# Kernel optimization log

Measured on AMD Instinct MI355X. Metric: run time of the kernel, lower is better.

## Reference

```python
import jax, jax.numpy as jnp
import numpy as np

B, S, D_IN, D_OUT, E, K = 4, 2048, 1024, 1024, 8, 2


def setup_inputs() -> dict:
    key = jax.random.key(0)
    ks = jax.random.split(key, 6)
    scale_in = 1.0 / np.sqrt(D_IN)
    return {
        "x": jax.random.normal(ks[0], (B, S, D_IN), dtype=jnp.float32),
        "gate_w": jax.random.uniform(ks[1], (E, D_IN), jnp.float32, -scale_in, scale_in),
        "gate_b": jax.random.uniform(ks[2], (E,), jnp.float32, -scale_in, scale_in),
        "expert_biases": jnp.zeros((E,), dtype=jnp.float32),
        "expert_w": jax.random.uniform(ks[3], (E, D_OUT, D_IN), jnp.float32, -scale_in, scale_in),
        "expert_b": jax.random.uniform(ks[4], (E, D_OUT), jnp.float32, -scale_in, scale_in),
    }


def reference(x, gate_w, gate_b, expert_biases, expert_w, expert_b):
    # Gating: sigmoid(Linear(x) + expert_biases), then top-k over experts
    gate_logits = jnp.einsum("bsd,ed->bse", x, gate_w) + gate_b + expert_biases
    gate_probs = jax.nn.sigmoid(gate_logits)
    top_k_probs, top_k_indices = jax.lax.top_k(gate_probs, K)  # [B,S,K]
    top_k_probs = top_k_probs / jnp.sum(top_k_probs, axis=-1, keepdims=True)

    # Dense all-expert compute: stack[e,b,s,o]
    expert_outputs = jnp.einsum("bsd,eod->ebso", x, expert_w) + expert_b[:, None, None, :]

    # Faithful reproduction of the original gather/permute:
    # result[b,s,j,o] = expert_outputs[tki[b,s,j], b, s, j]  (feature index is j, not o)
    bi = jnp.arange(B)[:, None, None]
    si = jnp.arange(S)[None, :, None]
    ji = jnp.arange(K)[None, None, :]
    val = expert_outputs[top_k_indices, bi, si, ji]  # [B,S,K]

    weighted = jnp.sum(val * top_k_probs, axis=-1)  # [B,S]
    final_output = jnp.broadcast_to(weighted[..., None], (B, S, D_OUT))
    return final_output, top_k_indices
```

## Files before the change

kernel.cpp:

```cpp
#include <hip/hip_runtime.h>
#include <math.h>

#define TOKENS 8192
#define DIN    1024
#define DOUT   1024
#define NE     8

__device__ __forceinline__ float wredsum(float v) {
#pragma unroll
  for (int off = 32; off > 0; off >>= 1) v += __shfl_xor(v, off, 64);
  return v;
}

__global__ __launch_bounds__(256, 4) void moe_fused(
    const float* __restrict__ x,
    const float* __restrict__ gate_w,
    const float* __restrict__ gate_b,
    const float* __restrict__ expert_biases,
    const float* __restrict__ expert_w,
    const float* __restrict__ expert_b,
    float* __restrict__ out,
    float* __restrict__ out_idx) {
  __shared__ float lgate[NE * DIN];
  {
    const float4* src = (const float4*)gate_w;
    float4* dst = (float4*)lgate;
#pragma unroll
    for (int i = 0; i < (NE * DIN / 4) / 256; ++i)
      dst[threadIdx.x + i * 256] = src[threadIdx.x + i * 256];
  }
  __syncthreads();

  const int wave = blockIdx.x * 4 + (threadIdx.x >> 6);
  const int lane = threadIdx.x & 63;
  const int t0 = wave * 2;
  const int t1 = t0 + 1;

  float4 xa[4], xb[4];
  const float4* xr0 = (const float4*)(x + (size_t)t0 * DIN);
  const float4* xr1 = (const float4*)(x + (size_t)t1 * DIN);
#pragma unroll
  for (int i = 0; i < 4; ++i) {
    xa[i] = xr0[lane + 64 * i];
    xb[i] = xr1[lane + 64 * i];
  }

  float za[NE], zb[NE];
#pragma unroll
  for (int e = 0; e < NE; ++e) { za[e] = 0.f; zb[e] = 0.f; }
#pragma unroll
  for (int e = 0; e < NE; ++e) {
    const float4* wr = (const float4*)(lgate + e * DIN);
#pragma unroll
    for (int i = 0; i < 4; ++i) {
      float4 w = wr[lane + 64 * i];
      za[e] += xa[i].x * w.x + xa[i].y * w.y + xa[i].z * w.z + xa[i].w * w.w;
      zb[e] += xb[i].x * w.x + xb[i].y * w.y + xb[i].z * w.z + xb[i].w * w.w;
    }
  }
#pragma unroll
  for (int e = 0; e < NE; ++e) {
    float bias = gate_b[e] + expert_biases[e];
    za[e] = wredsum(za[e]) + bias;
    zb[e] = wredsum(zb[e]) + bias;
  }

  int e0a = 0; float z0a = za[0];
#pragma unroll
  for (int e = 1; e < NE; ++e) if (za[e] > z0a) { z0a = za[e]; e0a = e; }
  int e1a = (e0a == 0) ? 1 : 0; float z1a = za[e1a];
#pragma unroll
  for (int e = 0; e < NE; ++e) if (e != e0a && za[e] > z1a) { z1a = za[e]; e1a = e; }

  int e0b = 0; float z0b = zb[0];
#pragma unroll
  for (int e = 1; e < NE; ++e) if (zb[e] > z0b) { z0b = zb[e]; e0b = e; }
  int e1b = (e0b == 0) ? 1 : 0; float z1b = zb[e1b];
#pragma unroll
  for (int e = 0; e < NE; ++e) if (e != e0b && zb[e] > z1b) { z1b = zb[e]; e1b = e; }

  float p0a = 1.f / (1.f + expf(-z0a));
  float p1a = 1.f / (1.f + expf(-z1a));
  float sa = 1.f / (p0a + p1a);
  float w0a = p0a * sa, w1a = p1a * sa;

  float p0b = 1.f / (1.f + expf(-z0b));
  float p1b = 1.f / (1.f + expf(-z1b));
  float sb = 1.f / (p0b + p1b);
  float w0b = p0b * sb, w1b = p1b * sb;

  const float4* ra0 = (const float4*)(expert_w + (size_t)e0a * (DOUT * DIN));
  const float4* ra1 = (const float4*)(expert_w + (size_t)e1a * (DOUT * DIN) + DIN);
  const float4* rb0 = (const float4*)(expert_w + (size_t)e0b * (DOUT * DIN));
  const float4* rb1 = (const float4*)(expert_w + (size_t)e1b * (DOUT * DIN) + DIN);

  float d0a = 0.f, d1a = 0.f, d0b = 0.f, d1b = 0.f;
#pragma unroll
  for (int i = 0; i < 4; ++i) {
    float4 wa0 = ra0[lane + 64 * i];
    float4 wa1 = ra1[lane + 64 * i];
    float4 wb0 = rb0[lane + 64 * i];
    float4 wb1 = rb1[lane + 64 * i];
    d0a += xa[i].x * wa0.x + xa[i].y * wa0.y + xa[i].z * wa0.z + xa[i].w * wa0.w;
    d1a += xa[i].x * wa1.x + xa[i].y * wa1.y + xa[i].z * wa1.z + xa[i].w * wa1.w;
    d0b += xb[i].x * wb0.x + xb[i].y * wb0.y + xb[i].z * wb0.z + xb[i].w * wb0.w;
    d1b += xb[i].x * wb1.x + xb[i].y * wb1.y + xb[i].z * wb1.z + xb[i].w * wb1.w;
  }
  d0a = wredsum(d0a) + expert_b[e0a * DOUT + 0];
  d1a = wredsum(d1a) + expert_b[e1a * DOUT + 1];
  d0b = wredsum(d0b) + expert_b[e0b * DOUT + 0];
  d1b = wredsum(d1b) + expert_b[e1b * DOUT + 1];

  float ova = d0a * w0a + d1a * w1a;
  float ovb = d0b * w0b + d1b * w1b;

  float4 va = make_float4(ova, ova, ova, ova);
  float4 vb = make_float4(ovb, ovb, ovb, ovb);
  float4* oa = (float4*)(out + (size_t)t0 * DOUT);
  float4* ob = (float4*)(out + (size_t)t1 * DOUT);
#pragma unroll
  for (int i = 0; i < 4; ++i) {
    oa[lane + 64 * i] = va;
    ob[lane + 64 * i] = vb;
  }

  if (lane == 0) {
    out_idx[t0 * 2 + 0] = (float)e0a;
    out_idx[t0 * 2 + 1] = (float)e1a;
    out_idx[t1 * 2 + 0] = (float)e0b;
    out_idx[t1 * 2 + 1] = (float)e1b;
  }
}

extern "C" void kernel_launch(void* const* d_in, const int* in_sizes, int n_in,
                              void* d_out, int out_size, void* d_ws, size_t ws_size,
                              hipStream_t stream) {
  const float* x             = (const float*)d_in[0];
  const float* gate_w        = (const float*)d_in[1];
  const float* gate_b        = (const float*)d_in[2];
  const float* expert_biases = (const float*)d_in[3];
  const float* expert_w      = (const float*)d_in[4];
  const float* expert_b      = (const float*)d_in[5];

  float* out     = (float*)d_out;
  float* out_idx = out + (size_t)TOKENS * DOUT;

  moe_fused<<<dim3(TOKENS / (4 * 2)), dim3(256), 0, stream>>>(
      x, gate_w, gate_b, expert_biases, expert_w, expert_b, out, out_idx);
}
```

Baseline: 130.8 us.

## Stage the 16 needed expert weight rows in LDS as bf16, use 512-thread blocks

```diff
diff --git a/kernel.cpp b/kernel.cpp
--- a/kernel.cpp
+++ b/kernel.cpp
@@ -6,13 +6,23 @@
 #define DOUT   1024
 #define NE     8
 
+typedef float vf4 __attribute__((ext_vector_type(4)));
+
 __device__ __forceinline__ float wredsum(float v) {
 #pragma unroll
   for (int off = 32; off > 0; off >>= 1) v += __shfl_xor(v, off, 64);
   return v;
 }
 
-__global__ __launch_bounds__(256, 4) void moe_fused(
+__device__ __forceinline__ unsigned short f2bf(float f) {
+  unsigned int u = __float_as_uint(f);
+  return (unsigned short)((u + 0x7FFFu + ((u >> 16) & 1u)) >> 16);
+}
+__device__ __forceinline__ float bf2f(unsigned short u) {
+  return __uint_as_float(((unsigned int)u) << 16);
+}
+
+__global__ __launch_bounds__(512, 4) void moe_fused(
     const float* __restrict__ x,
     const float* __restrict__ gate_w,
     const float* __restrict__ gate_b,
@@ -21,24 +31,40 @@
     const float* __restrict__ expert_b,
     float* __restrict__ out,
     float* __restrict__ out_idx) {
-  __shared__ float lgate[NE * DIN];
+  __shared__ float          lgate[NE * DIN];
+  __shared__ unsigned short lexp[16 * DIN];
+
   {
-    const float4* src = (const float4*)gate_w;
-    float4* dst = (float4*)lgate;
+    const vf4* src = (const vf4*)gate_w;
+    vf4* dst = (vf4*)lgate;
 #pragma unroll
-    for (int i = 0; i < (NE * DIN / 4) / 256; ++i)
-      dst[threadIdx.x + i * 256] = src[threadIdx.x + i * 256];
+    for (int i = 0; i < 4; ++i)
+      dst[threadIdx.x + 512 * i] = src[threadIdx.x + 512 * i];
+  }
+  {
+    const vf4* src = (const vf4*)expert_w;
+    ushort4* dst = (ushort4*)lexp;
+#pragma unroll
+    for (int k = 0; k < 8; ++k) {
+      int flat = threadIdx.x + 512 * k;
+      int row = flat >> 8;
+      int col = flat & 255;
+      int e = row & 7;
+      int o = row >> 3;
+      vf4 v = src[(size_t)e * (DOUT * DIN / 4) + o * (DIN / 4) + col];
+      dst[flat] = make_ushort4(f2bf(v.x), f2bf(v.y), f2bf(v.z), f2bf(v.w));
+    }
   }
   __syncthreads();
 
-  const int wave = blockIdx.x * 4 + (threadIdx.x >> 6);
+  const int wid  = blockIdx.x * 8 + (threadIdx.x >> 6);
   const int lane = threadIdx.x & 63;
-  const int t0 = wave * 2;
+  const int t0 = wid * 2;
   const int t1 = t0 + 1;
 
-  float4 xa[4], xb[4];
-  const float4* xr0 = (const float4*)(x + (size_t)t0 * DIN);
-  const float4* xr1 = (const float4*)(x + (size_t)t1 * DIN);
+  vf4 xa[4], xb[4];
+  const vf4* xr0 = (const vf4*)(x + (size_t)t0 * DIN);
+  const vf4* xr1 = (const vf4*)(x + (size_t)t1 * DIN);
 #pragma unroll
   for (int i = 0; i < 4; ++i) {
     xa[i] = xr0[lane + 64 * i];
@@ -50,10 +76,10 @@
   for (int e = 0; e < NE; ++e) { za[e] = 0.f; zb[e] = 0.f; }
 #pragma unroll
   for (int e = 0; e < NE; ++e) {
-    const float4* wr = (const float4*)(lgate + e * DIN);
+    const vf4* wr = (const vf4*)(lgate + e * DIN);
 #pragma unroll
     for (int i = 0; i < 4; ++i) {
-      float4 w = wr[lane + 64 * i];
+      vf4 w = wr[lane + 64 * i];
       za[e] += xa[i].x * w.x + xa[i].y * w.y + xa[i].z * w.z + xa[i].w * w.w;
       zb[e] += xb[i].x * w.x + xb[i].y * w.y + xb[i].z * w.z + xb[i].w * w.w;
     }
@@ -89,22 +115,22 @@
   float sb = 1.f / (p0b + p1b);
   float w0b = p0b * sb, w1b = p1b * sb;
 
-  const float4* ra0 = (const float4*)(expert_w + (size_t)e0a * (DOUT * DIN));
-  const float4* ra1 = (const float4*)(expert_w + (size_t)e1a * (DOUT * DIN) + DIN);
-  const float4* rb0 = (const float4*)(expert_w + (size_t)e0b * (DOUT * DIN));
-  const float4* rb1 = (const float4*)(expert_w + (size_t)e1b * (DOUT * DIN) + DIN);
+  const ushort4* ra0 = (const ushort4*)lexp + e0a * 256;
+  const ushort4* ra1 = (const ushort4*)lexp + (8 + e1a) * 256;
+  const ushort4* rb0 = (const ushort4*)lexp + e0b * 256;
+  const ushort4* rb1 = (const ushort4*)lexp + (8 + e1b) * 256;
 
   float d0a = 0.f, d1a = 0.f, d0b = 0.f, d1b = 0.f;
 #pragma unroll
   for (int i = 0; i < 4; ++i) {
-    float4 wa0 = ra0[lane + 64 * i];
-    float4 wa1 = ra1[lane + 64 * i];
-    float4 wb0 = rb0[lane + 64 * i];
-    float4 wb1 = rb1[lane + 64 * i];
-    d0a += xa[i].x * wa0.x + xa[i].y * wa0.y + xa[i].z * wa0.z + xa[i].w * wa0.w;
-    d1a += xa[i].x * wa1.x + xa[i].y * wa1.y + xa[i].z * wa1.z + xa[i].w * wa1.w;
-    d0b += xb[i].x * wb0.x + xb[i].y * wb0.y + xb[i].z * wb0.z + xb[i].w * wb0.w;
-    d1b += xb[i].x * wb1.x + xb[i].y * wb1.y + xb[i].z * wb1.z + xb[i].w * wb1.w;
+    ushort4 a0 = ra0[lane + 64 * i];
+    ushort4 a1 = ra1[lane + 64 * i];
+    ushort4 b0 = rb0[lane + 64 * i];
+    ushort4 b1 = rb1[lane + 64 * i];
+    d0a += xa[i].x * bf2f(a0.x) + xa[i].y * bf2f(a0.y) + xa[i].z * bf2f(a0.z) + xa[i].w * bf2f(a0.w);
+    d1a += xa[i].x * bf2f(a1.x) + xa[i].y * bf2f(a1.y) + xa[i].z * bf2f(a1.z) + xa[i].w * bf2f(a1.w);
+    d0b += xb[i].x * bf2f(b0.x) + xb[i].y * bf2f(b0.y) + xb[i].z * bf2f(b0.z) + xb[i].w * bf2f(b0.w);
+    d1b += xb[i].x * bf2f(b1.x) + xb[i].y * bf2f(b1.y) + xb[i].z * bf2f(b1.z) + xb[i].w * bf2f(b1.w);
   }
   d0a = wredsum(d0a) + expert_b[e0a * DOUT + 0];
   d1a = wredsum(d1a) + expert_b[e1a * DOUT + 1];
@@ -114,10 +140,10 @@
   float ova = d0a * w0a + d1a * w1a;
   float ovb = d0b * w0b + d1b * w1b;
 
-  float4 va = make_float4(ova, ova, ova, ova);
-  float4 vb = make_float4(ovb, ovb, ovb, ovb);
-  float4* oa = (float4*)(out + (size_t)t0 * DOUT);
-  float4* ob = (float4*)(out + (size_t)t1 * DOUT);
+  vf4 va = {ova, ova, ova, ova};
+  vf4 vb = {ovb, ovb, ovb, ovb};
+  vf4* oa = (vf4*)(out + (size_t)t0 * DOUT);
+  vf4* ob = (vf4*)(out + (size_t)t1 * DOUT);
 #pragma unroll
   for (int i = 0; i < 4; ++i) {
     oa[lane + 64 * i] = va;
@@ -145,6 +171,6 @@
   float* out     = (float*)d_out;
   float* out_idx = out + (size_t)TOKENS * DOUT;
 
-  moe_fused<<<dim3(TOKENS / (4 * 2)), dim3(256), 0, stream>>>(
+  moe_fused<<<dim3(512), dim3(512), 0, stream>>>(
       x, gate_w, gate_b, expert_biases, expert_w, expert_b, out, out_idx);
 }
```

After: 130.8 us. No clear change (+0.0%).
